# Optimization experiments

Hardware: AMD Instinct MI355X
Metric: run time of the kernel (lower is better)

The kernel has to match this reference:

```python
import jax, jax.numpy as jnp
import numpy as np

K1, K2 = 0.01, 0.03
DATA_RANGE = 1.0
EPS = 1e-6


def setup_inputs() -> dict:
    key = jax.random.key(0)
    k1, k2, k3 = jax.random.split(key, 3)
    B, C, H, W = 4, 3, 256, 176
    S, M = 5, 18
    X = jax.random.normal(k1, (B, C, H, W), dtype=jnp.float32)
    Y = jax.random.normal(k2, (B, C, H, W), dtype=jnp.float32)
    bp_mask = jax.random.uniform(k3, (B, S, M, H, W), dtype=jnp.float32)
    return {"X": X, "Y": Y, "bp_mask": bp_mask}


def reference(X, Y, bp_mask):
    # Rescale from [-1, 1] to [0, 1]
    X = (X + 1.0) / 2.0
    Y = (Y + 1.0) / 2.0
    C1 = (K1 * DATA_RANGE) ** 2
    C2 = (K2 * DATA_RANGE) ** 2

    # Normalized mask weights: [B, S, M, H, W]
    msum = bp_mask.sum(axis=(-2, -1), keepdims=True)
    w = bp_mask / (msum + EPS)

    # Masked first / second moments -> [B, S, M, C], no repeated 6D tensors
    mu1 = jnp.einsum('bchw,bsmhw->bsmc', X, w)
    mu2 = jnp.einsum('bchw,bsmhw->bsmc', Y, w)
    mu11 = jnp.einsum('bchw,bsmhw->bsmc', X * X, w)
    mu22 = jnp.einsum('bchw,bsmhw->bsmc', Y * Y, w)
    mu12 = jnp.einsum('bchw,bsmhw->bsmc', X * Y, w)

    mu1_sq = mu1 * mu1
    mu2_sq = mu2 * mu2
    mu1_mu2 = mu1 * mu2
    sigma1_sq = mu11 - mu1_sq
    sigma2_sq = mu22 - mu2_sq
    sigma12 = mu12 - mu1_mu2

    cs = (2.0 * sigma12 + C2) / (sigma1_sq + sigma2_sq + C2)
    ssim = (2.0 * mu1_mu2 + C1) / (mu1_sq + mu2_sq + C1) * cs
    # nonnegative_ssim=True
    ssim = jax.nn.relu(ssim)
    cs = jax.nn.relu(cs)

    # Mean over merged (M, C) axis -> [B, S]
    cs_batch = cs.mean(axis=(2, 3))
    ssim_batch = ssim.mean(axis=(2, 3))

    msssim = jnp.prod(cs_batch[:, :-1], axis=1) * ssim_batch[:, -1]
    return msssim.mean()
```

## Files before the change

### kernel.cpp

```cpp
#include <hip/hip_runtime.h>

#define B_  4
#define C_  3
#define S_  5
#define M_  18
#define HW  45056
#define HW4 (HW/4)
#define G   3
#define MG  (M_/G)
#define SPLIT 4
#define TPB 256
#define CHUNK4 (HW4/SPLIT)
#define ITERS (CHUNK4/TPB)
#define NGROUP (B_*S_*MG)
#define NBLK (NGROUP*SPLIT)
#define NPLANE (B_*S_*M_)

typedef float f4 __attribute__((ext_vector_type(4)));

__global__ __launch_bounds__(TPB, 2) void moments_kernel(
    const float4* __restrict__ X, const float4* __restrict__ Y,
    const f4* __restrict__ Mk, float* __restrict__ part) {
  int wg    = (blockIdx.x & 7) * (NBLK / 8) + (blockIdx.x >> 3);
  int group = wg / SPLIT;
  int chunk = wg - group * SPLIT;
  int bs    = group / MG;
  int mg    = group - bs * MG;
  int b     = bs / S_;

  const f4* mp0 = Mk + (size_t)(bs * M_ + mg * G + 0) * HW4;
  const f4* mp1 = Mk + (size_t)(bs * M_ + mg * G + 1) * HW4;
  const f4* mp2 = Mk + (size_t)(bs * M_ + mg * G + 2) * HW4;
  const float4* xp = X + (size_t)b * (C_ * HW4);
  const float4* yp = Y + (size_t)b * (C_ * HW4);

  int base = chunk * CHUNK4 + (int)threadIdx.x;

  float aW[G];
  float a1[G][C_], a2[G][C_], a11[G][C_], a22[G][C_], a12[G][C_];
#pragma unroll
  for (int g = 0; g < G; ++g) {
    aW[g] = 0.f;
#pragma unroll
    for (int c = 0; c < C_; ++c) {
      a1[g][c]=a2[g][c]=a11[g][c]=a22[g][c]=a12[g][c]=0.f;
    }
  }

#pragma unroll
  for (int it = 0; it < ITERS; ++it) {
    int i = base + it * TPB;
    f4 w0 = __builtin_nontemporal_load(mp0 + i);
    f4 w1 = __builtin_nontemporal_load(mp1 + i);
    f4 w2 = __builtin_nontemporal_load(mp2 + i);
    float wv[G][4] = {{w0.x,w0.y,w0.z,w0.w},
                      {w1.x,w1.y,w1.z,w1.w},
                      {w2.x,w2.y,w2.z,w2.w}};
    aW[0] += (w0.x + w0.y) + (w0.z + w0.w);
    aW[1] += (w1.x + w1.y) + (w1.z + w1.w);
    aW[2] += (w2.x + w2.y) + (w2.z + w2.w);
#pragma unroll
    for (int c = 0; c < C_; ++c) {
      float4 xv = xp[c * HW4 + i];
      float4 yv = yp[c * HW4 + i];
      float xvf[4] = {xv.x, xv.y, xv.z, xv.w};
      float yvf[4] = {yv.x, yv.y, yv.z, yv.w};
#pragma unroll
      for (int j = 0; j < 4; ++j) {
        float xc = xvf[j], yc = yvf[j];
        float xx = xc * xc, yy = yc * yc, xy = xc * yc;
#pragma unroll
        for (int g = 0; g < G; ++g) {
          float wc = wv[g][j];
          a1 [g][c] = fmaf(wc, xc, a1 [g][c]);
          a2 [g][c] = fmaf(wc, yc, a2 [g][c]);
          a11[g][c] = fmaf(wc, xx, a11[g][c]);
          a22[g][c] = fmaf(wc, yy, a22[g][c]);
          a12[g][c] = fmaf(wc, xy, a12[g][c]);
        }
      }
    }
  }

  float v[G*16];
#pragma unroll
  for (int g = 0; g < G; ++g) {
    v[g*16 + 0] = aW[g];
#pragma unroll
    for (int c = 0; c < C_; ++c) {
      v[g*16 + 1 + c*5 + 0] = a1 [g][c];
      v[g*16 + 1 + c*5 + 1] = a2 [g][c];
      v[g*16 + 1 + c*5 + 2] = a11[g][c];
      v[g*16 + 1 + c*5 + 3] = a22[g][c];
      v[g*16 + 1 + c*5 + 4] = a12[g][c];
    }
  }

#pragma unroll
  for (int off = 32; off > 0; off >>= 1) {
#pragma unroll
    for (int j = 0; j < G*16; ++j) v[j] += __shfl_xor(v[j], off);
  }

  __shared__ float red[TPB/64][G*16];
  int lane = threadIdx.x & 63;
  int wv_  = threadIdx.x >> 6;
  if (lane == 0) {
#pragma unroll
    for (int j = 0; j < G*16; ++j) red[wv_][j] = v[j];
  }
  __syncthreads();
  if (threadIdx.x < G*16) {
    float s = (red[0][threadIdx.x] + red[1][threadIdx.x]) +
              (red[2][threadIdx.x] + red[3][threadIdx.x]);
    part[(size_t)wg * (G*16) + threadIdx.x] = s;
  }
}

__global__ __launch_bounds__(384) void finalize_kernel(
    const float* __restrict__ part, float* __restrict__ out) {
  __shared__ float csS[NPLANE], ssS[NPLANE];
  __shared__ double csb[B_*S_], ssb[B_*S_];
  int t = threadIdx.x;

  if (t < NPLANE) {
    int bs = t / M_;
    int mrem = t - bs * M_;
    int mg = mrem / G;
    int g  = mrem - mg * G;
    int group = bs * MG + mg;

    double s[16];
#pragma unroll
    for (int j = 0; j < 16; ++j) s[j] = 0.0;
    for (int ch = 0; ch < SPLIT; ++ch) {
      const float* p = part + ((size_t)(group * SPLIT + ch) * G + g) * 16;
#pragma unroll
      for (int j = 0; j < 16; ++j) s[j] += (double)p[j];
    }
    const double C1d = 1e-4, C2d = 9e-4;
    double W = s[0];
    double inv = 1.0 / (W + 1e-6);
    double csAcc = 0.0, ssAcc = 0.0;
#pragma unroll
    for (int c = 0; c < C_; ++c) {
      double S1  = s[1 + c*5 + 0];
      double S2  = s[1 + c*5 + 1];
      double S11 = s[1 + c*5 + 2];
      double S22 = s[1 + c*5 + 3];
      double S12 = s[1 + c*5 + 4];
      double mu1  = (0.5*S1 + 0.5*W) * inv;
      double mu2  = (0.5*S2 + 0.5*W) * inv;
      double mu11 = (0.25*S11 + 0.5*S1 + 0.25*W) * inv;
      double mu22 = (0.25*S22 + 0.5*S2 + 0.25*W) * inv;
      double mu12 = (0.25*(S12 + S1 + S2 + W)) * inv;
      double m1s = mu1*mu1, m2s = mu2*mu2, m12 = mu1*mu2;
      double sig1  = mu11 - m1s;
      double sig2  = mu22 - m2s;
      double sig12 = mu12 - m12;
      double cs   = (2.0*sig12 + C2d) / (sig1 + sig2 + C2d);
      double ssim = (2.0*m12 + C1d) / (m1s + m2s + C1d) * cs;
      if (cs   < 0.0) cs   = 0.0;
      if (ssim < 0.0) ssim = 0.0;
      csAcc += cs; ssAcc += ssim;
    }
    csS[t] = (float)csAcc;
    ssS[t] = (float)ssAcc;
  }
  __syncthreads();

  if (t < B_*S_) {
    double cb = 0.0, sb = 0.0;
    for (int m = 0; m < M_; ++m) { cb += (double)csS[t*M_ + m]; sb += (double)ssS[t*M_ + m]; }
    csb[t] = cb / (double)(M_*C_);
    ssb[t] = sb / (double)(M_*C_);
  }
  __syncthreads();

  if (t == 0) {
    double acc = 0.0;
    for (int b = 0; b < B_; ++b) {
      double p = ssb[b*S_ + (S_-1)];
      for (int s = 0; s < S_-1; ++s) p *= csb[b*S_ + s];
      acc += p;
    }
    out[0] = (float)(acc / (double)B_);
  }
}

extern "C" void kernel_launch(void* const* d_in, const int* in_sizes, int n_in,
                              void* d_out, int out_size, void* d_ws, size_t ws_size,
                              hipStream_t stream) {
  (void)in_sizes; (void)n_in; (void)out_size; (void)ws_size;
  const float4* X  = (const float4*)d_in[0];
  const float4* Y  = (const float4*)d_in[1];
  const f4*     Mk = (const f4*)d_in[2];
  float* part = (float*)d_ws;
  float* out  = (float*)d_out;

  hipLaunchKernelGGL(moments_kernel, dim3(NBLK), dim3(TPB), 0, stream,
                     X, Y, Mk, part);
  hipLaunchKernelGGL(finalize_kernel, dim3(1), dim3(384), 0, stream, part, out);
}
```

Baseline: 122.9 us.

## Raise split count and replace shuffle reduction with LDS transpose reduction

Each (batch, scale, mask-group) plane is now split across 11 chunks instead of 4. This gives many more workgroups, so the GPU is better filled and memory latency is better hidden. The 48-value wavefront shuffle-xor reduction is replaced by one pass through LDS: every thread writes its partials to a 48 KB shared buffer, 192 threads each sum a quarter of the values for one slot, and a final small step combines the four quarters. The min-blocks hint is dropped from the launch bounds. The large LDS allocation may limit how many blocks fit on one CU, and the finalize kernel now reads more partial sums.

```diff
diff --git a/kernel.cpp b/kernel.cpp
--- a/kernel.cpp
+++ b/kernel.cpp
@@ -8,17 +8,18 @@
 #define HW4 (HW/4)
 #define G   3
 #define MG  (M_/G)
-#define SPLIT 4
+#define SPLIT 11
 #define TPB 256
 #define CHUNK4 (HW4/SPLIT)
 #define ITERS (CHUNK4/TPB)
 #define NGROUP (B_*S_*MG)
 #define NBLK (NGROUP*SPLIT)
 #define NPLANE (B_*S_*M_)
+#define NV (G*16)
 
 typedef float f4 __attribute__((ext_vector_type(4)));
 
-__global__ __launch_bounds__(TPB, 2) void moments_kernel(
+__global__ __launch_bounds__(TPB) void moments_kernel(
     const float4* __restrict__ X, const float4* __restrict__ Y,
     const f4* __restrict__ Mk, float* __restrict__ part) {
   int wg    = (blockIdx.x & 7) * (NBLK / 8) + (blockIdx.x >> 3);
@@ -82,7 +83,7 @@
     }
   }
 
-  float v[G*16];
+  float v[NV];
 #pragma unroll
   for (int g = 0; g < G; ++g) {
     v[g*16 + 0] = aW[g];
@@ -96,24 +97,32 @@
     }
   }
 
-#pragma unroll
-  for (int off = 32; off > 0; off >>= 1) {
-#pragma unroll
-    for (int j = 0; j < G*16; ++j) v[j] += __shfl_xor(v[j], off);
-  }
-
-  __shared__ float red[TPB/64][G*16];
-  int lane = threadIdx.x & 63;
-  int wv_  = threadIdx.x >> 6;
-  if (lane == 0) {
-#pragma unroll
-    for (int j = 0; j < G*16; ++j) red[wv_][j] = v[j];
-  }
-  __syncthreads();
-  if (threadIdx.x < G*16) {
-    float s = (red[0][threadIdx.x] + red[1][threadIdx.x]) +
-              (red[2][threadIdx.x] + red[3][threadIdx.x]);
-    part[(size_t)wg * (G*16) + threadIdx.x] = s;
+  __shared__ float4 ldsv[TPB * (NV/4)];
+#pragma unroll
+  for (int j4 = 0; j4 < NV/4; ++j4) {
+    float4 t;
+    t.x = v[j4*4+0]; t.y = v[j4*4+1]; t.z = v[j4*4+2]; t.w = v[j4*4+3];
+    ldsv[threadIdx.x * (NV/4) + j4] = t;
+  }
+  __syncthreads();
+
+  __shared__ float red2[4][NV];
+  const float* ldsf = (const float*)ldsv;
+  if (threadIdx.x < 4*NV) {
+    int slot = threadIdx.x % NV;
+    int q    = threadIdx.x / NV;
+    float s = 0.f;
+#pragma unroll
+    for (int k = 0; k < TPB/4; ++k) {
+      s += ldsf[(q*(TPB/4) + k) * NV + slot];
+    }
+    red2[q][slot] = s;
+  }
+  __syncthreads();
+  if (threadIdx.x < NV) {
+    float s = (red2[0][threadIdx.x] + red2[1][threadIdx.x]) +
+              (red2[2][threadIdx.x] + red2[3][threadIdx.x]);
+    part[(size_t)wg * NV + threadIdx.x] = s;
   }
 }
 
@@ -134,7 +143,7 @@
 #pragma unroll
     for (int j = 0; j < 16; ++j) s[j] = 0.0;
     for (int ch = 0; ch < SPLIT; ++ch) {
-      const float* p = part + ((size_t)(group * SPLIT + ch) * G + g) * 16;
+      const float* p = part + (size_t)(group * SPLIT + ch) * NV + g * 16;
 #pragma unroll
       for (int j = 0; j < 16; ++j) s[j] += (double)p[j];
     }
```

Measured after the change: 129.8 us. 1.06x slower.
